# Kernel optimization log

Hardware: AMD Instinct MI355X
Metric: run time of the kernel (lower is better)

## Reference

```python
import jax, jax.numpy as jnp
import numpy as np

PAD = 24
DR0, DR1 = 425.0, 905.0
DDIM = 128.0
N = 65536
H, W, D, FDIM = 176, 176, 132, 32
LAT, OUT, INP = 128, 257, 3
NUM_LAYERS = 8
SKIP = 4


def _linear_params(k, out_f, in_f):
    kw, kb = jax.random.split(k)
    s = 1.0 / np.sqrt(in_f)
    Wm = jax.random.uniform(kw, (out_f, in_f), jnp.float32, -s, s)
    bv = jax.random.uniform(kb, (out_f,), jnp.float32, -s, s)
    return Wm, bv


def setup_inputs() -> dict:
    key = jax.random.key(0)
    ks = jax.random.split(key, 20)
    world = jax.random.normal(ks[0], (N, 3), jnp.float32)
    u = jax.random.uniform(ks[1], (N,), jnp.float32, 2.0, 125.0)
    v = jax.random.uniform(ks[2], (N,), jnp.float32, 2.0, 125.0)
    d = jax.random.uniform(ks[3], (N,), jnp.float32, 440.0, 890.0)
    pixel = jnp.stack([u, v, d], axis=1)
    vol = jax.random.uniform(ks[4], (H, W, D, FDIM), jnp.float32)
    Wq, bq = _linear_params(ks[5], LAT, FDIM)
    inp = dict(sampled_points_world=world, sampled_points_pixel=pixel,
               feature_volume=vol, Wq=Wq, bq=bq)
    # MLP: layer0 3->128; layers 1..8: layer 4 is 128->125, else 128->128; layer9 128->257
    dims = [(LAT, INP)]
    for i in range(NUM_LAYERS):
        dims.append((LAT - INP if (i + 1) == SKIP else LAT, LAT))
    dims.append((OUT, LAT))
    for l, (o, i) in enumerate(dims):
        Wl, bl = _linear_params(ks[6 + l], o, i)
        inp[f"W{l}"] = Wl
        inp[f"b{l}"] = bl
    return inp


def softplus100(x):
    # torch Softplus(beta=100) with threshold=20: linear when 100*x > 20
    return jnp.where(x > 0.2, x, jnp.log1p(jnp.exp(jnp.minimum(x, 0.2) * 100.0)) / 100.0)


def query_layer(pixel, vol, Wq, bq):
    # q: padded/depth-normalized query coords [N,3]
    q = jnp.stack([pixel[:, 0] + PAD, pixel[:, 1] + PAD,
                   (pixel[:, 2] - DR0) / (DR1 - DR0) * DDIM], axis=1)
    base = jnp.floor(q).astype(jnp.int32)            # center = floor+0.5 for non-integer coords
    ax = jnp.arange(-1, 3)                           # window floor-1 .. floor+2 (4 per axis)
    offs = jnp.stack(jnp.meshgrid(ax, ax, ax, indexing='ij'), -1).reshape(-1, 3)  # [64,3]
    idx = base[:, None, :] + offs[None, :, :]        # [N,64,3]
    kcoord = idx.astype(q.dtype)
    vfeat = vol[idx[..., 0], idx[..., 1], idx[..., 2]]   # [N,64,F] gather
    sim = jnp.einsum('nkd,nd->nk', kcoord, q)            # key . query
    sim = sim / jnp.sum(sim, axis=1, keepdims=True)
    mixed = jnp.einsum('nk,nkf->nf', sim, vfeat)         # [N,F]
    feat = mixed / jnp.sum(mixed, axis=1, keepdims=True)
    return feat @ Wq.T + bq                              # [N,128]


def reference(sampled_points_world, sampled_points_pixel, feature_volume, Wq, bq,
              W0, b0, W1, b1, W2, b2, W3, b3, W4, b4,
              W5, b5, W6, b6, W7, b7, W8, b8, W9, b9):
    Ws = [W0, W1, W2, W3, W4, W5, W6, W7, W8, W9]
    bs = [b0, b1, b2, b3, b4, b5, b6, b7, b8, b9]
    bias = query_layer(sampled_points_pixel, feature_volume, Wq, bq)
    bias = bias / jnp.mean(jnp.abs(bias))
    x = sampled_points_world
    for l in range(NUM_LAYERS + 2):
        x = x @ Ws[l].T + bs[l]
        if l == SKIP:
            x = jnp.concatenate([x, sampled_points_world], axis=1)
        if l == 0:
            x = x * bias
        if l < NUM_LAYERS + 1:
            x = softplus100(x)
    return x
```

## Files before the change

### kernel.cpp

```cpp
#include <hip/hip_runtime.h>

#define NPTS 65536
#define VH 176
#define VW 176
#define VD 132
#define FD 32

typedef _Float16 half8 __attribute__((ext_vector_type(8)));
typedef float f32x4 __attribute__((ext_vector_type(4)));

struct Params {
    const float* W[10];
    const float* b[10];
};

__device__ __forceinline__ float sp100(float x) {
    if (x > 0.2f) return x;
    float e = __expf(x * 100.0f);
    return __logf(1.0f + e) * 0.01f;
}

__global__ __launch_bounds__(256) void query_kernel(
    const float* __restrict__ pixel, const float* __restrict__ vol,
    const float* __restrict__ Wq, const float* __restrict__ bq,
    float* __restrict__ feat_out, float* __restrict__ sum_abs)
{
    const int tid = threadIdx.x;
    const int f = tid & 31;
    const int p = blockIdx.x * 8 + (tid >> 5);

    const float qx = pixel[p*3+0] + 24.0f;
    const float qy = pixel[p*3+1] + 24.0f;
    const float qz = (pixel[p*3+2] - 425.0f) / 480.0f * 128.0f;
    const int bx = (int)floorf(qx);
    const int by = (int)floorf(qy);
    const int bz = (int)floorf(qz);

    float mixed = 0.0f;
    #pragma unroll
    for (int dx = 0; dx < 4; ++dx) {
        const int i0 = bx + dx - 1;
        const float sx = (float)i0 * qx;
        #pragma unroll
        for (int dy = 0; dy < 4; ++dy) {
            const int i1 = by + dy - 1;
            const int rowbase = (i0 * VW + i1) * VD;
            const float sxy = sx + (float)i1 * qy;
            #pragma unroll
            for (int dz = 0; dz < 4; ++dz) {
                const int i2 = bz + dz - 1;
                const float sim = sxy + (float)i2 * qz;
                const float v = vol[(rowbase + i2) * FD + f];
                mixed = fmaf(sim, v, mixed);
            }
        }
    }
    float tot = mixed;
    #pragma unroll
    for (int m = 16; m >= 1; m >>= 1) tot += __shfl_xor(tot, m, 32);
    const float feat = mixed / tot;
    feat_out[p*32 + f] = feat;

    float a0 = bq[f], a1 = bq[f+32], a2 = bq[f+64], a3 = bq[f+96];
    #pragma unroll
    for (int ff = 0; ff < 32; ++ff) {
        const float fv = __shfl(feat, ff, 32);
        a0 = fmaf(Wq[(f     )*32 + ff], fv, a0);
        a1 = fmaf(Wq[(f + 32)*32 + ff], fv, a1);
        a2 = fmaf(Wq[(f + 64)*32 + ff], fv, a2);
        a3 = fmaf(Wq[(f + 96)*32 + ff], fv, a3);
    }
    float s = fabsf(a0) + fabsf(a1) + fabsf(a2) + fabsf(a3);
    #pragma unroll
    for (int m = 32; m >= 1; m >>= 1) s += __shfl_xor(s, m, 64);
    __shared__ float part[4];
    if ((tid & 63) == 0) part[tid >> 6] = s;
    __syncthreads();
    if (tid == 0) atomicAdd(sum_abs, part[0] + part[1] + part[2] + part[3]);
}

__global__ __launch_bounds__(256) void mlp_kernel(
    const float* __restrict__ world, const float* __restrict__ feat,
    const float* __restrict__ Wq, const float* __restrict__ bq,
    const float* __restrict__ sum_abs, float* __restrict__ out, Params P)
{
    __shared__ __align__(16) _Float16 wbuf[128 * 136];
    __shared__ __align__(16) _Float16 act[64 * 136];
    __shared__ float bbuf[128];
    __shared__ float wld[64 * 4];
    __shared__ float wrow[128];

    const int tid = threadIdx.x;
    const int lane = tid & 63;
    const int wid = tid >> 6;
    const int m0 = blockIdx.x * 64;

    if (tid < 192) wld[(tid/3)*4 + (tid % 3)] = world[(m0 + tid/3)*3 + (tid % 3)];

    const float inv_mean = (float)NPTS * 128.0f / sum_abs[0];

    {
        const int m = tid >> 2;
        const int c0 = (tid & 3) * 32;
        float fv[32];
        #pragma unroll
        for (int i = 0; i < 32; ++i) fv[i] = feat[(m0 + m)*32 + i];
        const float wx = world[(m0+m)*3+0];
        const float wy = world[(m0+m)*3+1];
        const float wz = world[(m0+m)*3+2];
        for (int j = 0; j < 32; ++j) {
            const int c = c0 + j;
            float bias = bq[c];
            #pragma unroll
            for (int i = 0; i < 32; ++i) bias = fmaf(Wq[c*32 + i], fv[i], bias);
            const float h = P.b[0][c] + P.W[0][c*3+0]*wx + P.W[0][c*3+1]*wy + P.W[0][c*3+2]*wz;
            act[m*136 + c] = (_Float16)sp100(h * bias * inv_mean);
        }
    }

    const int ar = (wid*16 + (lane & 15)) * 136 + ((lane >> 4) * 8);
    const int brb = (lane & 15) * 136 + ((lane >> 4) * 8);
    const int erow = wid*16 + ((lane >> 4) * 4);
    const int ecol0 = lane & 15;

    #pragma unroll 1
    for (int l = 1; l <= 8; ++l) {
        const float* Wl = P.W[l];
        const float* bl = P.b[l];
        const int rows = (l == 4) ? 125 : 128;
        __syncthreads();
        #pragma unroll
        for (int i = tid; i < 4096; i += 256) {
            const int r = i >> 5;
            const int c4 = (i & 31) << 2;
            float4 w = make_float4(0.f, 0.f, 0.f, 0.f);
            if (r < rows) w = ((const float4*)Wl)[r*32 + (i & 31)];
            _Float16* d = &wbuf[r*136 + c4];
            d[0] = (_Float16)w.x; d[1] = (_Float16)w.y;
            d[2] = (_Float16)w.z; d[3] = (_Float16)w.w;
        }
        if (tid < 128) bbuf[tid] = (tid < rows) ? bl[tid] : 0.0f;
        __syncthreads();

        half8 a[4];
        #pragma unroll
        for (int c = 0; c < 4; ++c) a[c] = *(const half8*)&act[ar + c*32];

        f32x4 acc[8] = {};
        #pragma unroll
        for (int c = 0; c < 4; ++c) {
            #pragma unroll
            for (int ot = 0; ot < 8; ++ot) {
                const half8 bf = *(const half8*)&wbuf[brb + ot*16*136 + c*32];
                acc[ot] = __builtin_amdgcn_mfma_f32_16x16x32_f16(a[c], bf, acc[ot], 0, 0, 0);
            }
        }
        #pragma unroll
        for (int ot = 0; ot < 8; ++ot) {
            const int col = ot*16 + ecol0;
            #pragma unroll
            for (int r = 0; r < 4; ++r) {
                float v = acc[ot][r] + bbuf[col];
                if (l == 4 && col >= 125) v = wld[(erow + r)*4 + (col - 125)];
                act[(erow + r)*136 + col] = (_Float16)sp100(v);
            }
        }
    }

    #pragma unroll 1
    for (int hh = 0; hh < 2; ++hh) {
        __syncthreads();
        #pragma unroll
        for (int i = tid; i < 4096; i += 256) {
            const int r = i >> 5;
            const int c4 = (i & 31) << 2;
            const float4 w = ((const float4*)P.W[9])[(hh*128 + r)*32 + (i & 31)];
            _Float16* d = &wbuf[r*136 + c4];
            d[0] = (_Float16)w.x; d[1] = (_Float16)w.y;
            d[2] = (_Float16)w.z; d[3] = (_Float16)w.w;
        }
        if (tid < 128) bbuf[tid] = P.b[9][hh*128 + tid];
        __syncthreads();

        half8 a[4];
        #pragma unroll
        for (int c = 0; c < 4; ++c) a[c] = *(const half8*)&act[ar + c*32];

        f32x4 acc[8] = {};
        #pragma unroll
        for (int c = 0; c < 4; ++c) {
            #pragma unroll
            for (int ot = 0; ot < 8; ++ot) {
                const half8 bf = *(const half8*)&wbuf[brb + ot*16*136 + c*32];
                acc[ot] = __builtin_amdgcn_mfma_f32_16x16x32_f16(a[c], bf, acc[ot], 0, 0, 0);
            }
        }
        #pragma unroll
        for (int ot = 0; ot < 8; ++ot) {
            const int col = ot*16 + ecol0;
            #pragma unroll
            for (int r = 0; r < 4; ++r) {
                out[(size_t)(m0 + erow + r)*257 + hh*128 + col] = acc[ot][r] + bbuf[col];
            }
        }
    }

    __syncthreads();
    if (tid < 128) wrow[tid] = P.W[9][256*128 + tid];
    __syncthreads();
    if (tid < 64) {
        float s = P.b[9][256];
        #pragma unroll 16
        for (int k = 0; k < 128; ++k)
            s = fmaf((float)act[tid*136 + k], wrow[k], s);
        out[(size_t)(m0 + tid)*257 + 256] = s;
    }
}

extern "C" void kernel_launch(void* const* d_in, const int* in_sizes, int n_in,
                              void* d_out, int out_size, void* d_ws, size_t ws_size,
                              hipStream_t stream) {
    const float* world = (const float*)d_in[0];
    const float* pixel = (const float*)d_in[1];
    const float* vol   = (const float*)d_in[2];
    const float* Wq    = (const float*)d_in[3];
    const float* bq    = (const float*)d_in[4];
    Params P;
    for (int l = 0; l < 10; ++l) {
        P.W[l] = (const float*)d_in[5 + 2*l];
        P.b[l] = (const float*)d_in[6 + 2*l];
    }
    float* sum_abs = (float*)d_ws;
    float* featbuf = (float*)((char*)d_ws + 256);

    hipMemsetAsync(d_ws, 0, 256, stream);
    query_kernel<<<NPTS/8, 256, 0, stream>>>(pixel, vol, Wq, bq, featbuf, sum_abs);
    mlp_kernel<<<NPTS/64, 256, 0, stream>>>(world, featbuf, Wq, bq, sum_abs,
                                            (float*)d_out, P);
}
```

Measured before the change: 1.075 ms.

## Pre-convert weights to fp16 once and read MLP weights directly from global memory

Adds a prep kernel that converts all MLP and query weights to fp16 in workspace. The MLP kernel no longer stages each layer's weights into shared memory behind __syncthreads; each wave loads B fragments straight from global/L2 and works only on its own rows, which removes block barriers. The layer-0 bias projection now runs on MFMA using fp16 features, and the last output column is reduced with shuffles across all waves. Shared memory shrinks and launch bounds request 4 blocks per CU for higher occupancy, at the cost of repeated global weight reads per wave and lower precision in the feature path.

New measurement: 926.6 us. 13.8% less time.

```diff
diff --git a/kernel.cpp b/kernel.cpp
--- a/kernel.cpp
+++ b/kernel.cpp
@@ -1,13 +1,17 @@
 #include <hip/hip_runtime.h>
 
 #define NPTS 65536
-#define VH 176
 #define VW 176
 #define VD 132
 #define FD 32
 
 typedef _Float16 half8 __attribute__((ext_vector_type(8)));
 typedef float f32x4 __attribute__((ext_vector_type(4)));
+
+#define OFF_WQ 0
+#define OFF_L1 4096
+#define OFF_L9 (4096 + 8 * 16384)
+#define W16_TOTAL (4096 + 8 * 16384 + 32768)
 
 struct Params {
     const float* W[10];
@@ -20,10 +24,29 @@
     return __logf(1.0f + e) * 0.01f;
 }
 
+__global__ __launch_bounds__(256) void prep_kernel(Params P, const float* __restrict__ Wq,
+                                                   _Float16* __restrict__ w16) {
+    const int i = blockIdx.x * 256 + threadIdx.x;
+    if (i >= W16_TOTAL) return;
+    if (i < 4096) { w16[i] = (_Float16)Wq[i]; return; }
+    int j = i - 4096;
+    if (j < 8 * 16384) {
+        const int l = (j >> 14) + 1;
+        const int r = (j & 16383) >> 7;
+        float v = 0.0f;
+        if (l != 4) v = P.W[l][j & 16383];
+        else if (r < 125) v = P.W[4][j & 16383];
+        w16[i] = (_Float16)v;
+        return;
+    }
+    j -= 8 * 16384;
+    w16[i] = (_Float16)P.W[9][j];
+}
+
 __global__ __launch_bounds__(256) void query_kernel(
     const float* __restrict__ pixel, const float* __restrict__ vol,
     const float* __restrict__ Wq, const float* __restrict__ bq,
-    float* __restrict__ feat_out, float* __restrict__ sum_abs)
+    _Float16* __restrict__ feat_out, float* __restrict__ sum_abs)
 {
     const int tid = threadIdx.x;
     const int f = tid & 31;
@@ -36,7 +59,7 @@
     const int by = (int)floorf(qy);
     const int bz = (int)floorf(qz);
 
-    float mixed = 0.0f;
+    float mix0 = 0.0f, mix1 = 0.0f;
     #pragma unroll
     for (int dx = 0; dx < 4; ++dx) {
         const int i0 = bx + dx - 1;
@@ -51,15 +74,17 @@
                 const int i2 = bz + dz - 1;
                 const float sim = sxy + (float)i2 * qz;
                 const float v = vol[(rowbase + i2) * FD + f];
-                mixed = fmaf(sim, v, mixed);
-            }
-        }
-    }
+                if (dx < 2) mix0 = fmaf(sim, v, mix0);
+                else        mix1 = fmaf(sim, v, mix1);
+            }
+        }
+    }
+    const float mixed = mix0 + mix1;
     float tot = mixed;
     #pragma unroll
     for (int m = 16; m >= 1; m >>= 1) tot += __shfl_xor(tot, m, 32);
     const float feat = mixed / tot;
-    feat_out[p*32 + f] = feat;
+    feat_out[p*32 + f] = (_Float16)feat;
 
     float a0 = bq[f], a1 = bq[f+32], a2 = bq[f+64], a3 = bq[f+96];
     #pragma unroll
@@ -79,141 +104,130 @@
     if (tid == 0) atomicAdd(sum_abs, part[0] + part[1] + part[2] + part[3]);
 }
 
-__global__ __launch_bounds__(256) void mlp_kernel(
-    const float* __restrict__ world, const float* __restrict__ feat,
-    const float* __restrict__ Wq, const float* __restrict__ bq,
+__global__ __launch_bounds__(256, 4) void mlp_kernel(
+    const float* __restrict__ world, const _Float16* __restrict__ feat16,
+    const _Float16* __restrict__ w16, const float* __restrict__ bq,
     const float* __restrict__ sum_abs, float* __restrict__ out, Params P)
 {
-    __shared__ __align__(16) _Float16 wbuf[128 * 136];
     __shared__ __align__(16) _Float16 act[64 * 136];
-    __shared__ float bbuf[128];
-    __shared__ float wld[64 * 4];
-    __shared__ float wrow[128];
-
-    const int tid = threadIdx.x;
+
+    const int tid  = threadIdx.x;
     const int lane = tid & 63;
-    const int wid = tid >> 6;
-    const int m0 = blockIdx.x * 64;
-
-    if (tid < 192) wld[(tid/3)*4 + (tid % 3)] = world[(m0 + tid/3)*3 + (tid % 3)];
-
+    const int wid  = tid >> 6;
+    const int n16  = lane & 15;
+    const int kg   = lane >> 4;
+    const int wrow0 = wid * 16;
+    const int gm    = blockIdx.x * 64 + wrow0;
     const float inv_mean = (float)NPTS * 128.0f / sum_abs[0];
 
     {
-        const int m = tid >> 2;
-        const int c0 = (tid & 3) * 32;
-        float fv[32];
-        #pragma unroll
-        for (int i = 0; i < 32; ++i) fv[i] = feat[(m0 + m)*32 + i];
-        const float wx = world[(m0+m)*3+0];
-        const float wy = world[(m0+m)*3+1];
-        const float wz = world[(m0+m)*3+2];
-        for (int j = 0; j < 32; ++j) {
-            const int c = c0 + j;
-            float bias = bq[c];
-            #pragma unroll
-            for (int i = 0; i < 32; ++i) bias = fmaf(Wq[c*32 + i], fv[i], bias);
-            const float h = P.b[0][c] + P.W[0][c*3+0]*wx + P.W[0][c*3+1]*wy + P.W[0][c*3+2]*wz;
-            act[m*136 + c] = (_Float16)sp100(h * bias * inv_mean);
-        }
-    }
-
-    const int ar = (wid*16 + (lane & 15)) * 136 + ((lane >> 4) * 8);
-    const int brb = (lane & 15) * 136 + ((lane >> 4) * 8);
-    const int erow = wid*16 + ((lane >> 4) * 4);
-    const int ecol0 = lane & 15;
+        const half8 fa = *(const half8*)&feat16[(size_t)(gm + n16) * 32 + kg * 8];
+        f32x4 acc[8];
+        #pragma unroll
+        for (int ot = 0; ot < 8; ++ot) {
+            const half8 bf = *(const half8*)&w16[OFF_WQ + (ot*16 + n16) * 32 + kg * 8];
+            f32x4 z = {};
+            acc[ot] = __builtin_amdgcn_mfma_f32_16x16x32_f16(fa, bf, z, 0, 0, 0);
+        }
+        float w0x[8], w0y[8], w0z[8], b0a[8], bqa[8];
+        #pragma unroll
+        for (int ot = 0; ot < 8; ++ot) {
+            const int col = ot*16 + n16;
+            w0x[ot] = P.W[0][col*3+0]; w0y[ot] = P.W[0][col*3+1]; w0z[ot] = P.W[0][col*3+2];
+            b0a[ot] = P.b[0][col];     bqa[ot] = bq[col];
+        }
+        #pragma unroll
+        for (int r = 0; r < 4; ++r) {
+            const int row = kg*4 + r;
+            const float wx = world[(gm+row)*3+0];
+            const float wy = world[(gm+row)*3+1];
+            const float wz = world[(gm+row)*3+2];
+            #pragma unroll
+            for (int ot = 0; ot < 8; ++ot) {
+                const float h = b0a[ot] + w0x[ot]*wx + w0y[ot]*wy + w0z[ot]*wz;
+                const float bias = acc[ot][r] + bqa[ot];
+                act[(wrow0+row)*136 + ot*16 + n16] = (_Float16)sp100(h * bias * inv_mean);
+            }
+        }
+    }
+
+    const int a_off = (wrow0 + n16) * 136 + kg * 8;
 
     #pragma unroll 1
     for (int l = 1; l <= 8; ++l) {
-        const float* Wl = P.W[l];
-        const float* bl = P.b[l];
-        const int rows = (l == 4) ? 125 : 128;
-        __syncthreads();
-        #pragma unroll
-        for (int i = tid; i < 4096; i += 256) {
-            const int r = i >> 5;
-            const int c4 = (i & 31) << 2;
-            float4 w = make_float4(0.f, 0.f, 0.f, 0.f);
-            if (r < rows) w = ((const float4*)Wl)[r*32 + (i & 31)];
-            _Float16* d = &wbuf[r*136 + c4];
-            d[0] = (_Float16)w.x; d[1] = (_Float16)w.y;
-            d[2] = (_Float16)w.z; d[3] = (_Float16)w.w;
-        }
-        if (tid < 128) bbuf[tid] = (tid < rows) ? bl[tid] : 0.0f;
-        __syncthreads();
-
+        const _Float16* wl = &w16[OFF_L1 + (l - 1) * 16384];
         half8 a[4];
         #pragma unroll
-        for (int c = 0; c < 4; ++c) a[c] = *(const half8*)&act[ar + c*32];
+        for (int c = 0; c < 4; ++c) a[c] = *(const half8*)&act[a_off + c*32];
 
         f32x4 acc[8] = {};
         #pragma unroll
         for (int c = 0; c < 4; ++c) {
             #pragma unroll
             for (int ot = 0; ot < 8; ++ot) {
-                const half8 bf = *(const half8*)&wbuf[brb + ot*16*136 + c*32];
+                const half8 bf = *(const half8*)&wl[(ot*16 + n16)*128 + kg*8 + c*32];
                 acc[ot] = __builtin_amdgcn_mfma_f32_16x16x32_f16(a[c], bf, acc[ot], 0, 0, 0);
             }
         }
-        #pragma unroll
-        for (int ot = 0; ot < 8; ++ot) {
-            const int col = ot*16 + ecol0;
+        const bool l4 = (l == 4);
+        float blv[8];
+        #pragma unroll
+        for (int ot = 0; ot < 8; ++ot) {
+            const int col = ot*16 + n16;
+            blv[ot] = (l4 && col >= 125) ? 0.0f : P.b[l][col];
+        }
+        #pragma unroll
+        for (int ot = 0; ot < 8; ++ot) {
+            const int col = ot*16 + n16;
             #pragma unroll
             for (int r = 0; r < 4; ++r) {
-                float v = acc[ot][r] + bbuf[col];
-                if (l == 4 && col >= 125) v = wld[(erow + r)*4 + (col - 125)];
-                act[(erow + r)*136 + col] = (_Float16)sp100(v);
-            }
-        }
-    }
-
-    #pragma unroll 1
-    for (int hh = 0; hh < 2; ++hh) {
-        __syncthreads();
-        #pragma unroll
-        for (int i = tid; i < 4096; i += 256) {
-            const int r = i >> 5;
-            const int c4 = (i & 31) << 2;
-            const float4 w = ((const float4*)P.W[9])[(hh*128 + r)*32 + (i & 31)];
-            _Float16* d = &wbuf[r*136 + c4];
-            d[0] = (_Float16)w.x; d[1] = (_Float16)w.y;
-            d[2] = (_Float16)w.z; d[3] = (_Float16)w.w;
-        }
-        if (tid < 128) bbuf[tid] = P.b[9][hh*128 + tid];
-        __syncthreads();
-
+                const int row = kg*4 + r;
+                float v = acc[ot][r] + blv[ot];
+                if (l4 && col >= 125) v = world[(gm+row)*3 + (col - 125)];
+                act[(wrow0+row)*136 + col] = (_Float16)sp100(v);
+            }
+        }
+    }
+
+    {
         half8 a[4];
         #pragma unroll
-        for (int c = 0; c < 4; ++c) a[c] = *(const half8*)&act[ar + c*32];
-
-        f32x4 acc[8] = {};
-        #pragma unroll
-        for (int c = 0; c < 4; ++c) {
+        for (int c = 0; c < 4; ++c) a[c] = *(const half8*)&act[a_off + c*32];
+
+        #pragma unroll 1
+        for (int hh = 0; hh < 2; ++hh) {
+            f32x4 acc[8] = {};
+            #pragma unroll
+            for (int c = 0; c < 4; ++c) {
+                #pragma unroll
+                for (int ot = 0; ot < 8; ++ot) {
+                    const half8 bf = *(const half8*)&w16[OFF_L9 + (hh*128 + ot*16 + n16)*128 + kg*8 + c*32];
+                    acc[ot] = __builtin_amdgcn_mfma_f32_16x16x32_f16(a[c], bf, acc[ot], 0, 0, 0);
+                }
+            }
             #pragma unroll
             for (int ot = 0; ot < 8; ++ot) {
-                const half8 bf = *(const half8*)&wbuf[brb + ot*16*136 + c*32];
-                acc[ot] = __builtin_amdgcn_mfma_f32_16x16x32_f16(a[c], bf, acc[ot], 0, 0, 0);
-            }
-        }
-        #pragma unroll
-        for (int ot = 0; ot < 8; ++ot) {
-            const int col = ot*16 + ecol0;
-            #pragma unroll
-            for (int r = 0; r < 4; ++r) {
-                out[(size_t)(m0 + erow + r)*257 + hh*128 + col] = acc[ot][r] + bbuf[col];
-            }
-        }
-    }
-
-    __syncthreads();
-    if (tid < 128) wrow[tid] = P.W[9][256*128 + tid];
-    __syncthreads();
-    if (tid < 64) {
-        float s = P.b[9][256];
-        #pragma unroll 16
-        for (int k = 0; k < 128; ++k)
-            s = fmaf((float)act[tid*136 + k], wrow[k], s);
-        out[(size_t)(m0 + tid)*257 + 256] = s;
+                const int col = ot*16 + n16;
+                const float b9 = P.b[9][hh*128 + col];
+                #pragma unroll
+                for (int r = 0; r < 4; ++r) {
+                    out[(size_t)(gm + kg*4 + r)*257 + hh*128 + col] = acc[ot][r] + b9;
+                }
+            }
+        }
+    }
+    {
+        const int rr = lane >> 2;
+        const int q  = lane & 3;
+        float s = 0.0f;
+        #pragma unroll
+        for (int j = 0; j < 32; ++j) {
+            const int k = q*32 + j;
+            s = fmaf((float)act[(wrow0 + rr)*136 + k], P.W[9][256*128 + k], s);
+        }
+        s += __shfl_xor(s, 1, 64);
+        s += __shfl_xor(s, 2, 64);
+        if (q == 0) out[(size_t)(gm + rr)*257 + 256] = P.b[9][256] + s;
     }
 }
 
@@ -230,11 +244,13 @@
         P.W[l] = (const float*)d_in[5 + 2*l];
         P.b[l] = (const float*)d_in[6 + 2*l];
     }
-    float* sum_abs = (float*)d_ws;
-    float* featbuf = (float*)((char*)d_ws + 256);
+    float*    sum_abs = (float*)d_ws;
+    _Float16* feat16  = (_Float16*)((char*)d_ws + 4096);
+    _Float16* w16     = (_Float16*)((char*)d_ws + 4096 + (size_t)NPTS * 32 * 2);
 
     hipMemsetAsync(d_ws, 0, 256, stream);
-    query_kernel<<<NPTS/8, 256, 0, stream>>>(pixel, vol, Wq, bq, featbuf, sum_abs);
-    mlp_kernel<<<NPTS/64, 256, 0, stream>>>(world, featbuf, Wq, bq, sum_abs,
-                                            (float*)d_out, P);
-}
+    prep_kernel<<<(W16_TOTAL + 255) / 256, 256, 0, stream>>>(P, Wq, w16);
+    query_kernel<<<NPTS / 8, 256, 0, stream>>>(pixel, vol, Wq, bq, feat16, sum_abs);
+    mlp_kernel<<<NPTS / 64, 256, 0, stream>>>(world, feat16, w16, bq, sum_abs,
+                                              (float*)d_out, P);
+}
```
